# Optimization experiments

Hardware: AMD Instinct MI355X
Metric: run time of the kernel (lower is better)

Reference implementation:

```python
import jax, jax.numpy as jnp
import numpy as np

N, D, H, G = 262144, 256, 8, 2048
DH = D // H  # 32


def setup_inputs() -> dict:
    key = jax.random.key(0)
    ks = jax.random.split(key, 12)
    s = 0.02
    x = jax.random.normal(ks[0], (N, D), jnp.float32)
    # equal-size sets: batch[i] = set id, ptr = CSR boundaries (consistent pair)
    batch = jnp.repeat(jnp.arange(G, dtype=jnp.int64), N // G)
    ptr = jnp.arange(G + 1, dtype=jnp.int64) * (N // G)
    rn = lambda k, sh: jax.random.normal(k, sh, jnp.float32) * s
    return {
        "x": x, "ptr": ptr, "batch": batch,
        "lin_w": rn(ks[1], (D, D)), "lin_b": jnp.zeros((D,), jnp.float32),
        "seed": rn(ks[2], (D,)),
        "wq": rn(ks[3], (D, D)), "bq": jnp.zeros((D,), jnp.float32),
        "wk": rn(ks[4], (D, D)), "bk": jnp.zeros((D,), jnp.float32),
        "wv": rn(ks[5], (D, D)), "bv": jnp.zeros((D,), jnp.float32),
        "wo": rn(ks[6], (D, D)), "bo": jnp.zeros((D,), jnp.float32),
        "mlp_w1": rn(ks[7], (D, D)), "mlp_b1": jnp.zeros((D,), jnp.float32),
        "mlp_w2": rn(ks[8], (D, D)), "mlp_b2": jnp.zeros((D,), jnp.float32),
    }


def gelu(v):
    return jax.nn.gelu(v, approximate=False)  # torch nn.GELU default (erf)


def reference(x, ptr, batch, lin_w, lin_b, seed, wq, bq, wk, bk, wv, bv,
              wo, bo, mlp_w1, mlp_b1, mlp_w2, mlp_b2):
    # pre-projection + GELU
    h = gelu(x @ lin_w + lin_b)                         # [N, D]
    # PMA-style multihead attention pooling over ragged sets
    q = (seed @ wq + bq).reshape(H, DH)                 # learnable seed query per head
    k = (h @ wk + bk).reshape(-1, H, DH)                # [N, H, DH]
    v = (h @ wv + bv).reshape(-1, H, DH)                # [N, H, DH]
    scores = jnp.einsum('nhd,hd->nh', k, q) / jnp.sqrt(jnp.float32(DH))  # [N, H]
    # segment (per-set) numerically-stable softmax
    m = jax.ops.segment_max(scores, batch, num_segments=G)   # [G, H]
    e = jnp.exp(scores - m[batch])
    z = jax.ops.segment_sum(e, batch, num_segments=G)        # [G, H]
    w = e / z[batch]                                         # [N, H] attention weights
    pooled = jax.ops.segment_sum(w[:, :, None] * v, batch, num_segments=G)  # [G, H, DH]
    pooled = pooled.reshape(G, D) @ wo + bo                  # output projection [G, D]
    # 2-layer MLP head (plain_last: no act on final layer; dropout=0 at eval)
    out = gelu(pooled @ mlp_w1 + mlp_b1) @ mlp_w2 + mlp_b2   # [G, D]
    return out
```

## Files before the change

kernel.cpp:

```cpp
#include <hip/hip_runtime.h>
#include <hip/hip_bf16.h>

#define DD 256
#define SETSZ 128
#define NSETS 2048

typedef __attribute__((ext_vector_type(8))) __bf16 bf16x8;
typedef __attribute__((ext_vector_type(8))) unsigned short u16x8;
typedef __attribute__((ext_vector_type(4))) float f32x4;

static __device__ __forceinline__ unsigned short f2bf(float f) {
    unsigned u = __builtin_bit_cast(unsigned, f);
    u += 0x7fffu + ((u >> 16) & 1u);
    return (unsigned short)(u >> 16);
}

static __device__ __forceinline__ float gelu_f(float v) {
    return 0.5f * v * (1.0f + erff(v * 0.70710678118654752f));
}

__global__ void prep1_kernel(const float* __restrict__ seed, const float* __restrict__ wq,
                             const float* __restrict__ bq, float* __restrict__ q) {
    int j = threadIdx.x;
    float s = bq[j];
#pragma unroll 16
    for (int d = 0; d < DD; ++d) s += seed[d] * wq[d * DD + j];
    q[j] = s;
}

__global__ void prep2_kernel(const float* __restrict__ lin_w, const float* __restrict__ wv,
                             const float* __restrict__ wk, const float* __restrict__ q,
                             unsigned short* __restrict__ linT, unsigned short* __restrict__ wvT,
                             unsigned short* __restrict__ wkqB) {
    int b = blockIdx.x, t = threadIdx.x;
    if (b < DD) {
        linT[b * DD + t] = f2bf(lin_w[t * DD + b]);
        wvT[b * DD + t]  = f2bf(wv[t * DD + b]);
    } else {
        const float inv = 0.17677669529663687f;
        for (int c = 0; c < 8; ++c) {
            float s = 0.f;
#pragma unroll 8
            for (int j = 0; j < 32; ++j) s += wk[t * DD + c * 32 + j] * q[c * 32 + j];
            wkqB[c * DD + t] = f2bf(s * inv);
        }
        for (int c = 8; c < 16; ++c) wkqB[c * DD + t] = 0;
    }
}

__global__ __launch_bounds__(512, 2)
void attn_pool_kernel(const float* __restrict__ x, const float* __restrict__ lin_b,
                      const float* __restrict__ bv,
                      const unsigned short* __restrict__ linT,
                      const unsigned short* __restrict__ wvT,
                      const unsigned short* __restrict__ wkqB,
                      float* __restrict__ pooled) {
    __shared__ unsigned short xs[SETSZ * DD];
    const int g = blockIdx.x;
    const int t = threadIdx.x;
    const int lane = t & 63;
    const int wid = t >> 6;
    const int l15 = lane & 15;
    const int kg = lane >> 4;
    const long r0 = (long)g * SETSZ;

#pragma unroll
    for (int i = 0; i < 8; ++i) {
        int c = i * 512 + t;
        int row = c >> 5;
        int cg = c & 31;
        const float4* src = reinterpret_cast<const float4*>(x + (r0 + row) * DD + cg * 8);
        float4 a0 = src[0];
        float4 a1 = src[1];
        u16x8 v;
        v[0] = f2bf(a0.x); v[1] = f2bf(a0.y); v[2] = f2bf(a0.z); v[3] = f2bf(a0.w);
        v[4] = f2bf(a1.x); v[5] = f2bf(a1.y); v[6] = f2bf(a1.z); v[7] = f2bf(a1.w);
        int sg = cg ^ (row & 7);
        *reinterpret_cast<u16x8*>(&xs[row * DD + sg * 8]) = v;
    }
    __syncthreads();

    const int colbase = wid * 32;

    f32x4 acc[8][2];
#pragma unroll
    for (int r = 0; r < 8; ++r) { acc[r][0] = 0.f; acc[r][1] = 0.f; }

#pragma unroll
    for (int ks = 0; ks < 8; ++ks) {
        bf16x8 af[8];
#pragma unroll
        for (int r = 0; r < 8; ++r) {
            int row = r * 16 + l15;
            int sg = (ks * 4 + kg) ^ (row & 7);
            af[r] = *reinterpret_cast<const bf16x8*>(&xs[row * DD + sg * 8]);
        }
        int bofs = ks * 32 + kg * 8;
        bf16x8 b0 = *reinterpret_cast<const bf16x8*>(linT + (colbase + l15) * DD + bofs);
        bf16x8 b1 = *reinterpret_cast<const bf16x8*>(linT + (colbase + 16 + l15) * DD + bofs);
#pragma unroll
        for (int r = 0; r < 8; ++r) {
            acc[r][0] = __builtin_amdgcn_mfma_f32_16x16x32_bf16(af[r], b0, acc[r][0], 0, 0, 0);
            acc[r][1] = __builtin_amdgcn_mfma_f32_16x16x32_bf16(af[r], b1, acc[r][1], 0, 0, 0);
        }
    }
    __syncthreads();

    {
        float lb0 = lin_b[colbase + l15];
        float lb1 = lin_b[colbase + 16 + l15];
#pragma unroll
        for (int r = 0; r < 8; ++r) {
#pragma unroll
            for (int c = 0; c < 2; ++c) {
                int col = colbase + c * 16 + l15;
                float lb = c ? lb1 : lb0;
#pragma unroll
                for (int j = 0; j < 4; ++j) {
                    int row = r * 16 + kg * 4 + j;
                    float hv = gelu_f(acc[r][c][j] + lb);
                    int sg = (col >> 3) ^ (row & 7);
                    xs[row * DD + sg * 8 + (col & 7)] = f2bf(hv);
                }
            }
        }
    }
    __syncthreads();

    f32x4 vacc[8][2];
    f32x4 sacc[8];
#pragma unroll
    for (int r = 0; r < 8; ++r) { vacc[r][0] = 0.f; vacc[r][1] = 0.f; sacc[r] = 0.f; }

#pragma unroll
    for (int ks = 0; ks < 8; ++ks) {
        bf16x8 af[8];
#pragma unroll
        for (int r = 0; r < 8; ++r) {
            int row = r * 16 + l15;
            int sg = (ks * 4 + kg) ^ (row & 7);
            af[r] = *reinterpret_cast<const bf16x8*>(&xs[row * DD + sg * 8]);
        }
        int bofs = ks * 32 + kg * 8;
        bf16x8 b0 = *reinterpret_cast<const bf16x8*>(wvT + (colbase + l15) * DD + bofs);
        bf16x8 b1 = *reinterpret_cast<const bf16x8*>(wvT + (colbase + 16 + l15) * DD + bofs);
        bf16x8 bq8 = *reinterpret_cast<const bf16x8*>(wkqB + l15 * DD + bofs);
#pragma unroll
        for (int r = 0; r < 8; ++r) {
            vacc[r][0] = __builtin_amdgcn_mfma_f32_16x16x32_bf16(af[r], b0, vacc[r][0], 0, 0, 0);
            vacc[r][1] = __builtin_amdgcn_mfma_f32_16x16x32_bf16(af[r], b1, vacc[r][1], 0, 0, 0);
            sacc[r]    = __builtin_amdgcn_mfma_f32_16x16x32_bf16(af[r], bq8, sacc[r], 0, 0, 0);
        }
    }

    float e[8][4];
    float mx = -1e30f;
#pragma unroll
    for (int r = 0; r < 8; ++r)
#pragma unroll
        for (int j = 0; j < 4; ++j) {
            float s = __shfl(sacc[r][j], (lane & 48) | wid, 64);
            e[r][j] = s;
            mx = fmaxf(mx, s);
        }
    mx = fmaxf(mx, __shfl_xor(mx, 16, 64));
    mx = fmaxf(mx, __shfl_xor(mx, 32, 64));
    float z = 0.f;
#pragma unroll
    for (int r = 0; r < 8; ++r)
#pragma unroll
        for (int j = 0; j < 4; ++j) {
            float ee = __expf(e[r][j] - mx);
            e[r][j] = ee;
            z += ee;
        }
    z += __shfl_xor(z, 16, 64);
    z += __shfl_xor(z, 32, 64);
    float inv = 1.0f / z;

#pragma unroll
    for (int c = 0; c < 2; ++c) {
        float pp = 0.f;
#pragma unroll
        for (int r = 0; r < 8; ++r)
#pragma unroll
            for (int j = 0; j < 4; ++j) pp += e[r][j] * vacc[r][c][j];
        pp *= inv;
        pp += __shfl_xor(pp, 16, 64);
        pp += __shfl_xor(pp, 32, 64);
        if (kg == 0) {
            int col = colbase + c * 16 + l15;
            pooled[(long)g * DD + col] = pp + bv[col];
        }
    }
}

__global__ __launch_bounds__(256)
void mlp_kernel(const float* __restrict__ pooled,
                const float* __restrict__ wo, const float* __restrict__ bo,
                const float* __restrict__ w1, const float* __restrict__ b1,
                const float* __restrict__ w2, const float* __restrict__ b2,
                float* __restrict__ out) {
    __shared__ float sa[8][DD];
    __shared__ float sb[8][DD];
    const int c = threadIdx.x;
    const long base = (long)blockIdx.x * 8 * DD;
#pragma unroll
    for (int r = 0; r < 8; ++r) sa[r][c] = pooled[base + r * DD + c];
    __syncthreads();
    {
        float acc[8];
        float bb = bo[c];
#pragma unroll
        for (int r = 0; r < 8; ++r) acc[r] = bb;
#pragma unroll 4
        for (int k = 0; k < DD; ++k) {
            float wvv = wo[k * DD + c];
#pragma unroll
            for (int r = 0; r < 8; ++r) acc[r] += sa[r][k] * wvv;
        }
#pragma unroll
        for (int r = 0; r < 8; ++r) sb[r][c] = acc[r];
    }
    __syncthreads();
    {
        float acc[8];
        float bb = b1[c];
#pragma unroll
        for (int r = 0; r < 8; ++r) acc[r] = bb;
#pragma unroll 4
        for (int k = 0; k < DD; ++k) {
            float wvv = w1[k * DD + c];
#pragma unroll
            for (int r = 0; r < 8; ++r) acc[r] += sb[r][k] * wvv;
        }
#pragma unroll
        for (int r = 0; r < 8; ++r) sa[r][c] = gelu_f(acc[r]);
    }
    __syncthreads();
    {
        float acc[8];
        float bb = b2[c];
#pragma unroll
        for (int r = 0; r < 8; ++r) acc[r] = bb;
#pragma unroll 4
        for (int k = 0; k < DD; ++k) {
            float wvv = w2[k * DD + c];
#pragma unroll
            for (int r = 0; r < 8; ++r) acc[r] += sa[r][k] * wvv;
        }
#pragma unroll
        for (int r = 0; r < 8; ++r) out[base + r * DD + c] = acc[r];
    }
}

extern "C" void kernel_launch(void* const* d_in, const int* in_sizes, int n_in,
                              void* d_out, int out_size, void* d_ws, size_t ws_size,
                              hipStream_t stream) {
    const float* x     = (const float*)d_in[0];
    const float* lin_w = (const float*)d_in[3];
    const float* lin_b = (const float*)d_in[4];
    const float* seed  = (const float*)d_in[5];
    const float* wq    = (const float*)d_in[6];
    const float* bq    = (const float*)d_in[7];
    const float* wk    = (const float*)d_in[8];
    const float* wvp   = (const float*)d_in[10];
    const float* bv    = (const float*)d_in[11];
    const float* wo    = (const float*)d_in[12];
    const float* bo    = (const float*)d_in[13];
    const float* w1    = (const float*)d_in[14];
    const float* b1    = (const float*)d_in[15];
    const float* w2    = (const float*)d_in[16];
    const float* b2    = (const float*)d_in[17];
    float* out = (float*)d_out;

    char* ws = (char*)d_ws;
    float* q             = (float*)ws;
    unsigned short* wkqB = (unsigned short*)(ws + 4096);
    unsigned short* linT = (unsigned short*)(ws + 16384);
    unsigned short* wvT  = (unsigned short*)(ws + 16384 + 131072);
    float* pooled        = (float*)(ws + 16384 + 262144);

    prep1_kernel<<<1, 256, 0, stream>>>(seed, wq, bq, q);
    prep2_kernel<<<257, 256, 0, stream>>>(lin_w, wvp, wk, q, linT, wvT, wkqB);
    attn_pool_kernel<<<NSETS, 512, 0, stream>>>(x, lin_b, bv, linT, wvT, wkqB, pooled);
    mlp_kernel<<<NSETS / 8, 256, 0, stream>>>(pooled, wo, bo, w1, b1, w2, b2, out);
}
```

Baseline: 250.7 us.

## Tile attention-pool over 32-row chunks with online softmax and register prefetch

The attention-pool kernel now processes each 128-row set in four 32-row tiles instead of staging the whole set in LDS. The 64 KB LDS buffer shrinks to 16 KB, and launch bounds rise to allow 6 blocks per CU. Each tile accumulates the softmax with a running max and rescaling (online softmax), and the next tile's x is prefetched into registers while the current tile computes. In exchange the kernel does more barriers per block, runs a smaller MFMA batch per iteration, and exposes load latency per tile. It also uses an extra XOR term in the LDS swizzle.

```diff
diff --git a/kernel.cpp b/kernel.cpp
--- a/kernel.cpp
+++ b/kernel.cpp
@@ -3,6 +3,8 @@
 
 #define DD 256
 #define SETSZ 128
+#define TROWS 32
+#define NTILES 4
 #define NSETS 2048
 
 typedef __attribute__((ext_vector_type(8))) __bf16 bf16x8;
@@ -17,6 +19,10 @@
 
 static __device__ __forceinline__ float gelu_f(float v) {
     return 0.5f * v * (1.0f + erff(v * 0.70710678118654752f));
+}
+
+static __device__ __forceinline__ int swz(int row, int cg) {
+    return cg ^ (row & 7) ^ ((row >> 3) & 3);
 }
 
 __global__ void prep1_kernel(const float* __restrict__ seed, const float* __restrict__ wq,
@@ -48,14 +54,14 @@
     }
 }
 
-__global__ __launch_bounds__(512, 2)
+__global__ __launch_bounds__(512, 6)
 void attn_pool_kernel(const float* __restrict__ x, const float* __restrict__ lin_b,
                       const float* __restrict__ bv,
                       const unsigned short* __restrict__ linT,
                       const unsigned short* __restrict__ wvT,
                       const unsigned short* __restrict__ wkqB,
                       float* __restrict__ pooled) {
-    __shared__ unsigned short xs[SETSZ * DD];
+    __shared__ unsigned short xs[TROWS * DD];
     const int g = blockIdx.x;
     const int t = threadIdx.x;
     const int lane = t & 63;
@@ -63,135 +69,162 @@
     const int l15 = lane & 15;
     const int kg = lane >> 4;
     const long r0 = (long)g * SETSZ;
-
-#pragma unroll
-    for (int i = 0; i < 8; ++i) {
-        int c = i * 512 + t;
-        int row = c >> 5;
-        int cg = c & 31;
-        const float4* src = reinterpret_cast<const float4*>(x + (r0 + row) * DD + cg * 8);
-        float4 a0 = src[0];
-        float4 a1 = src[1];
-        u16x8 v;
-        v[0] = f2bf(a0.x); v[1] = f2bf(a0.y); v[2] = f2bf(a0.z); v[3] = f2bf(a0.w);
-        v[4] = f2bf(a1.x); v[5] = f2bf(a1.y); v[6] = f2bf(a1.z); v[7] = f2bf(a1.w);
-        int sg = cg ^ (row & 7);
-        *reinterpret_cast<u16x8*>(&xs[row * DD + sg * 8]) = v;
+    const int colbase = wid * 32;
+
+    const int srow0 = t >> 5;
+    const int srow1 = srow0 + 16;
+    const int scg = t & 31;
+    const int soff0 = srow0 * DD + swz(srow0, scg) * 8;
+    const int soff1 = srow1 * DD + swz(srow1, scg) * 8;
+
+    const float lb0 = lin_b[colbase + l15];
+    const float lb1 = lin_b[colbase + 16 + l15];
+
+    float m = -1e30f, z = 0.f, pp0 = 0.f, pp1 = 0.f;
+
+    {
+        const float* p0 = x + (r0 + srow0) * DD + scg * 8;
+        const float* p1 = x + (r0 + srow1) * DD + scg * 8;
+        float4 a0 = *(const float4*)p0;
+        float4 a1 = *(const float4*)(p0 + 4);
+        float4 c0 = *(const float4*)p1;
+        float4 c1 = *(const float4*)(p1 + 4);
+        u16x8 v0, v1;
+        v0[0]=f2bf(a0.x); v0[1]=f2bf(a0.y); v0[2]=f2bf(a0.z); v0[3]=f2bf(a0.w);
+        v0[4]=f2bf(a1.x); v0[5]=f2bf(a1.y); v0[6]=f2bf(a1.z); v0[7]=f2bf(a1.w);
+        v1[0]=f2bf(c0.x); v1[1]=f2bf(c0.y); v1[2]=f2bf(c0.z); v1[3]=f2bf(c0.w);
+        v1[4]=f2bf(c1.x); v1[5]=f2bf(c1.y); v1[6]=f2bf(c1.z); v1[7]=f2bf(c1.w);
+        *reinterpret_cast<u16x8*>(&xs[soff0]) = v0;
+        *reinterpret_cast<u16x8*>(&xs[soff1]) = v1;
     }
     __syncthreads();
 
-    const int colbase = wid * 32;
-
-    f32x4 acc[8][2];
-#pragma unroll
-    for (int r = 0; r < 8; ++r) { acc[r][0] = 0.f; acc[r][1] = 0.f; }
-
-#pragma unroll
-    for (int ks = 0; ks < 8; ++ks) {
-        bf16x8 af[8];
-#pragma unroll
-        for (int r = 0; r < 8; ++r) {
-            int row = r * 16 + l15;
-            int sg = (ks * 4 + kg) ^ (row & 7);
-            af[r] = *reinterpret_cast<const bf16x8*>(&xs[row * DD + sg * 8]);
-        }
-        int bofs = ks * 32 + kg * 8;
-        bf16x8 b0 = *reinterpret_cast<const bf16x8*>(linT + (colbase + l15) * DD + bofs);
-        bf16x8 b1 = *reinterpret_cast<const bf16x8*>(linT + (colbase + 16 + l15) * DD + bofs);
-#pragma unroll
-        for (int r = 0; r < 8; ++r) {
-            acc[r][0] = __builtin_amdgcn_mfma_f32_16x16x32_bf16(af[r], b0, acc[r][0], 0, 0, 0);
-            acc[r][1] = __builtin_amdgcn_mfma_f32_16x16x32_bf16(af[r], b1, acc[r][1], 0, 0, 0);
-        }
-    }
-    __syncthreads();
-
-    {
-        float lb0 = lin_b[colbase + l15];
-        float lb1 = lin_b[colbase + 16 + l15];
-#pragma unroll
-        for (int r = 0; r < 8; ++r) {
+#pragma unroll 1
+    for (int tl = 0; tl < NTILES; ++tl) {
+        float4 pf0, pf1, pf2, pf3;
+        if (tl < NTILES - 1) {
+            const float* p0 = x + (r0 + (tl + 1) * TROWS + srow0) * DD + scg * 8;
+            const float* p1 = x + (r0 + (tl + 1) * TROWS + srow1) * DD + scg * 8;
+            pf0 = *(const float4*)p0;
+            pf1 = *(const float4*)(p0 + 4);
+            pf2 = *(const float4*)p1;
+            pf3 = *(const float4*)(p1 + 4);
+        }
+
+        f32x4 acc[2][2];
+        acc[0][0] = 0.f; acc[0][1] = 0.f; acc[1][0] = 0.f; acc[1][1] = 0.f;
+#pragma unroll 2
+        for (int ks = 0; ks < 8; ++ks) {
+            bf16x8 af[2];
+#pragma unroll
+            for (int rr = 0; rr < 2; ++rr) {
+                int row = rr * 16 + l15;
+                af[rr] = *reinterpret_cast<const bf16x8*>(&xs[row * DD + swz(row, ks * 4 + kg) * 8]);
+            }
+            int bofs = ks * 32 + kg * 8;
+            bf16x8 b0 = *reinterpret_cast<const bf16x8*>(linT + (colbase + l15) * DD + bofs);
+            bf16x8 b1 = *reinterpret_cast<const bf16x8*>(linT + (colbase + 16 + l15) * DD + bofs);
+#pragma unroll
+            for (int rr = 0; rr < 2; ++rr) {
+                acc[rr][0] = __builtin_amdgcn_mfma_f32_16x16x32_bf16(af[rr], b0, acc[rr][0], 0, 0, 0);
+                acc[rr][1] = __builtin_amdgcn_mfma_f32_16x16x32_bf16(af[rr], b1, acc[rr][1], 0, 0, 0);
+            }
+        }
+        __syncthreads();
+
+#pragma unroll
+        for (int rr = 0; rr < 2; ++rr) {
 #pragma unroll
             for (int c = 0; c < 2; ++c) {
                 int col = colbase + c * 16 + l15;
                 float lb = c ? lb1 : lb0;
 #pragma unroll
                 for (int j = 0; j < 4; ++j) {
-                    int row = r * 16 + kg * 4 + j;
-                    float hv = gelu_f(acc[r][c][j] + lb);
-                    int sg = (col >> 3) ^ (row & 7);
-                    xs[row * DD + sg * 8 + (col & 7)] = f2bf(hv);
+                    int row = rr * 16 + kg * 4 + j;
+                    float hv = gelu_f(acc[rr][c][j] + lb);
+                    xs[row * DD + swz(row, col >> 3) * 8 + (col & 7)] = f2bf(hv);
                 }
             }
         }
-    }
-    __syncthreads();
-
-    f32x4 vacc[8][2];
-    f32x4 sacc[8];
-#pragma unroll
-    for (int r = 0; r < 8; ++r) { vacc[r][0] = 0.f; vacc[r][1] = 0.f; sacc[r] = 0.f; }
-
-#pragma unroll
-    for (int ks = 0; ks < 8; ++ks) {
-        bf16x8 af[8];
-#pragma unroll
-        for (int r = 0; r < 8; ++r) {
-            int row = r * 16 + l15;
-            int sg = (ks * 4 + kg) ^ (row & 7);
-            af[r] = *reinterpret_cast<const bf16x8*>(&xs[row * DD + sg * 8]);
-        }
-        int bofs = ks * 32 + kg * 8;
-        bf16x8 b0 = *reinterpret_cast<const bf16x8*>(wvT + (colbase + l15) * DD + bofs);
-        bf16x8 b1 = *reinterpret_cast<const bf16x8*>(wvT + (colbase + 16 + l15) * DD + bofs);
-        bf16x8 bq8 = *reinterpret_cast<const bf16x8*>(wkqB + l15 * DD + bofs);
-#pragma unroll
-        for (int r = 0; r < 8; ++r) {
-            vacc[r][0] = __builtin_amdgcn_mfma_f32_16x16x32_bf16(af[r], b0, vacc[r][0], 0, 0, 0);
-            vacc[r][1] = __builtin_amdgcn_mfma_f32_16x16x32_bf16(af[r], b1, vacc[r][1], 0, 0, 0);
-            sacc[r]    = __builtin_amdgcn_mfma_f32_16x16x32_bf16(af[r], bq8, sacc[r], 0, 0, 0);
-        }
-    }
-
-    float e[8][4];
-    float mx = -1e30f;
-#pragma unroll
-    for (int r = 0; r < 8; ++r)
-#pragma unroll
-        for (int j = 0; j < 4; ++j) {
-            float s = __shfl(sacc[r][j], (lane & 48) | wid, 64);
-            e[r][j] = s;
-            mx = fmaxf(mx, s);
-        }
-    mx = fmaxf(mx, __shfl_xor(mx, 16, 64));
-    mx = fmaxf(mx, __shfl_xor(mx, 32, 64));
-    float z = 0.f;
-#pragma unroll
-    for (int r = 0; r < 8; ++r)
-#pragma unroll
-        for (int j = 0; j < 4; ++j) {
-            float ee = __expf(e[r][j] - mx);
-            e[r][j] = ee;
-            z += ee;
-        }
+        __syncthreads();
+
+        f32x4 vacc[2][2];
+        f32x4 sacc[2];
+        vacc[0][0] = 0.f; vacc[0][1] = 0.f; vacc[1][0] = 0.f; vacc[1][1] = 0.f;
+        sacc[0] = 0.f; sacc[1] = 0.f;
+#pragma unroll 2
+        for (int ks = 0; ks < 8; ++ks) {
+            bf16x8 af[2];
+#pragma unroll
+            for (int rr = 0; rr < 2; ++rr) {
+                int row = rr * 16 + l15;
+                af[rr] = *reinterpret_cast<const bf16x8*>(&xs[row * DD + swz(row, ks * 4 + kg) * 8]);
+            }
+            int bofs = ks * 32 + kg * 8;
+            bf16x8 b0  = *reinterpret_cast<const bf16x8*>(wvT + (colbase + l15) * DD + bofs);
+            bf16x8 b1  = *reinterpret_cast<const bf16x8*>(wvT + (colbase + 16 + l15) * DD + bofs);
+            bf16x8 bq8 = *reinterpret_cast<const bf16x8*>(wkqB + l15 * DD + bofs);
+#pragma unroll
+            for (int rr = 0; rr < 2; ++rr) {
+                vacc[rr][0] = __builtin_amdgcn_mfma_f32_16x16x32_bf16(af[rr], b0, vacc[rr][0], 0, 0, 0);
+                vacc[rr][1] = __builtin_amdgcn_mfma_f32_16x16x32_bf16(af[rr], b1, vacc[rr][1], 0, 0, 0);
+                sacc[rr]    = __builtin_amdgcn_mfma_f32_16x16x32_bf16(af[rr], bq8, sacc[rr], 0, 0, 0);
+            }
+        }
+        __syncthreads();
+
+        {
+            float sv[2][4];
+            float tm = -1e30f;
+#pragma unroll
+            for (int rr = 0; rr < 2; ++rr)
+#pragma unroll
+                for (int j = 0; j < 4; ++j) {
+                    float s = __shfl(sacc[rr][j], (lane & 48) | wid, 64);
+                    sv[rr][j] = s;
+                    tm = fmaxf(tm, s);
+                }
+            tm = fmaxf(tm, __shfl_xor(tm, 16, 64));
+            tm = fmaxf(tm, __shfl_xor(tm, 32, 64));
+            float mnew = fmaxf(m, tm);
+            float al = __expf(m - mnew);
+            z *= al; pp0 *= al; pp1 *= al;
+#pragma unroll
+            for (int rr = 0; rr < 2; ++rr)
+#pragma unroll
+                for (int j = 0; j < 4; ++j) {
+                    float e = __expf(sv[rr][j] - mnew);
+                    z += e;
+                    pp0 += e * vacc[rr][0][j];
+                    pp1 += e * vacc[rr][1][j];
+                }
+            m = mnew;
+        }
+
+        if (tl < NTILES - 1) {
+            u16x8 v0, v1;
+            v0[0]=f2bf(pf0.x); v0[1]=f2bf(pf0.y); v0[2]=f2bf(pf0.z); v0[3]=f2bf(pf0.w);
+            v0[4]=f2bf(pf1.x); v0[5]=f2bf(pf1.y); v0[6]=f2bf(pf1.z); v0[7]=f2bf(pf1.w);
+            v1[0]=f2bf(pf2.x); v1[1]=f2bf(pf2.y); v1[2]=f2bf(pf2.z); v1[3]=f2bf(pf2.w);
+            v1[4]=f2bf(pf3.x); v1[5]=f2bf(pf3.y); v1[6]=f2bf(pf3.z); v1[7]=f2bf(pf3.w);
+            *reinterpret_cast<u16x8*>(&xs[soff0]) = v0;
+            *reinterpret_cast<u16x8*>(&xs[soff1]) = v1;
+        }
+        __syncthreads();
+    }
+
     z += __shfl_xor(z, 16, 64);
     z += __shfl_xor(z, 32, 64);
+    pp0 += __shfl_xor(pp0, 16, 64);
+    pp0 += __shfl_xor(pp0, 32, 64);
+    pp1 += __shfl_xor(pp1, 16, 64);
+    pp1 += __shfl_xor(pp1, 32, 64);
     float inv = 1.0f / z;
-
-#pragma unroll
-    for (int c = 0; c < 2; ++c) {
-        float pp = 0.f;
-#pragma unroll
-        for (int r = 0; r < 8; ++r)
-#pragma unroll
-            for (int j = 0; j < 4; ++j) pp += e[r][j] * vacc[r][c][j];
-        pp *= inv;
-        pp += __shfl_xor(pp, 16, 64);
-        pp += __shfl_xor(pp, 32, 64);
-        if (kg == 0) {
-            int col = colbase + c * 16 + l15;
-            pooled[(long)g * DD + col] = pp + bv[col];
-        }
+    if (kg == 0) {
+        int c0 = colbase + l15;
+        int c1 = colbase + 16 + l15;
+        pooled[(long)g * DD + c0] = pp0 * inv + bv[c0];
+        pooled[(long)g * DD + c1] = pp1 * inv + bv[c1];
     }
 }
 
```

Result: slower. 525.7 us (+109.7%).

## Make attention-pool kernel persistent with double-buffered LDS and register prefetch

Applied to the files above, without the earlier changes.

Launches 256 persistent blocks, each processing 8 sets in sequence. While the MFMAs for the current set run, each block loads the next set's x into registers and writes it as bf16 into a second LDS buffer, so global loads overlap compute. The LDS swizzle also gains an extra XOR term to reduce bank conflicts. In exchange, doubling LDS to 128 KB per block drops residency to one block per CU, and the prefetch registers add pressure under the existing launch bounds, which may cause spills.

```diff
diff --git a/kernel.cpp b/kernel.cpp
--- a/kernel.cpp
+++ b/kernel.cpp
@@ -4,6 +4,8 @@
 #define DD 256
 #define SETSZ 128
 #define NSETS 2048
+#define NBLK 256
+#define SPB (NSETS / NBLK)
 
 typedef __attribute__((ext_vector_type(8))) __bf16 bf16x8;
 typedef __attribute__((ext_vector_type(8))) unsigned short u16x8;
@@ -18,6 +20,15 @@
 static __device__ __forceinline__ float gelu_f(float v) {
     return 0.5f * v * (1.0f + erff(v * 0.70710678118654752f));
 }
+
+static __device__ __forceinline__ int swz(int row, int cg) {
+    return cg ^ (row & 7) ^ ((row >> 3) & 3);
+}
+
+#define LGKM_BARRIER() do { \
+    asm volatile("s_waitcnt lgkmcnt(0)" ::: "memory"); \
+    __builtin_amdgcn_s_barrier(); \
+} while (0)
 
 __global__ void prep1_kernel(const float* __restrict__ seed, const float* __restrict__ wq,
                              const float* __restrict__ bq, float* __restrict__ q) {
@@ -55,143 +66,183 @@
                       const unsigned short* __restrict__ wvT,
                       const unsigned short* __restrict__ wkqB,
                       float* __restrict__ pooled) {
-    __shared__ unsigned short xs[SETSZ * DD];
-    const int g = blockIdx.x;
+    __shared__ unsigned short bufs[2][SETSZ * DD];
     const int t = threadIdx.x;
     const int lane = t & 63;
     const int wid = t >> 6;
     const int l15 = lane & 15;
     const int kg = lane >> 4;
-    const long r0 = (long)g * SETSZ;
-
-#pragma unroll
-    for (int i = 0; i < 8; ++i) {
-        int c = i * 512 + t;
-        int row = c >> 5;
-        int cg = c & 31;
-        const float4* src = reinterpret_cast<const float4*>(x + (r0 + row) * DD + cg * 8);
-        float4 a0 = src[0];
-        float4 a1 = src[1];
+    const int colbase = wid * 32;
+    const long set0 = (long)blockIdx.x * SPB;
+
+    const float lb0 = lin_b[colbase + l15];
+    const float lb1 = lin_b[colbase + 16 + l15];
+
+    auto issueg = [&](const float* nb, int g, float4* pr) {
+        const float4* src = reinterpret_cast<const float4*>(nb);
+        int c0 = g * 2048 + 2 * t;
+        pr[0] = src[c0];
+        pr[1] = src[c0 + 1];
+        pr[2] = src[c0 + 1024];
+        pr[3] = src[c0 + 1025];
+    };
+    auto writeg = [&](unsigned short* dst, int g, const float4* pr) {
+        int c0 = g * 2048 + 2 * t;
+        int row = c0 >> 6;
+        int cg = (c0 & 63) >> 1;
         u16x8 v;
-        v[0] = f2bf(a0.x); v[1] = f2bf(a0.y); v[2] = f2bf(a0.z); v[3] = f2bf(a0.w);
-        v[4] = f2bf(a1.x); v[5] = f2bf(a1.y); v[6] = f2bf(a1.z); v[7] = f2bf(a1.w);
-        int sg = cg ^ (row & 7);
-        *reinterpret_cast<u16x8*>(&xs[row * DD + sg * 8]) = v;
-    }
-    __syncthreads();
-
-    const int colbase = wid * 32;
-
-    f32x4 acc[8][2];
-#pragma unroll
-    for (int r = 0; r < 8; ++r) { acc[r][0] = 0.f; acc[r][1] = 0.f; }
-
-#pragma unroll
-    for (int ks = 0; ks < 8; ++ks) {
-        bf16x8 af[8];
-#pragma unroll
-        for (int r = 0; r < 8; ++r) {
-            int row = r * 16 + l15;
-            int sg = (ks * 4 + kg) ^ (row & 7);
-            af[r] = *reinterpret_cast<const bf16x8*>(&xs[row * DD + sg * 8]);
-        }
-        int bofs = ks * 32 + kg * 8;
-        bf16x8 b0 = *reinterpret_cast<const bf16x8*>(linT + (colbase + l15) * DD + bofs);
-        bf16x8 b1 = *reinterpret_cast<const bf16x8*>(linT + (colbase + 16 + l15) * DD + bofs);
-#pragma unroll
-        for (int r = 0; r < 8; ++r) {
-            acc[r][0] = __builtin_amdgcn_mfma_f32_16x16x32_bf16(af[r], b0, acc[r][0], 0, 0, 0);
-            acc[r][1] = __builtin_amdgcn_mfma_f32_16x16x32_bf16(af[r], b1, acc[r][1], 0, 0, 0);
-        }
-    }
-    __syncthreads();
+        v[0] = f2bf(pr[0].x); v[1] = f2bf(pr[0].y); v[2] = f2bf(pr[0].z); v[3] = f2bf(pr[0].w);
+        v[4] = f2bf(pr[1].x); v[5] = f2bf(pr[1].y); v[6] = f2bf(pr[1].z); v[7] = f2bf(pr[1].w);
+        *reinterpret_cast<u16x8*>(&dst[row * DD + swz(row, cg) * 8]) = v;
+        int row2 = row + 16;
+        u16x8 w;
+        w[0] = f2bf(pr[2].x); w[1] = f2bf(pr[2].y); w[2] = f2bf(pr[2].z); w[3] = f2bf(pr[2].w);
+        w[4] = f2bf(pr[3].x); w[5] = f2bf(pr[3].y); w[6] = f2bf(pr[3].z); w[7] = f2bf(pr[3].w);
+        *reinterpret_cast<u16x8*>(&dst[row2 * DD + swz(row2, cg) * 8]) = w;
+    };
 
     {
-        float lb0 = lin_b[colbase + l15];
-        float lb1 = lin_b[colbase + 16 + l15];
-#pragma unroll
-        for (int r = 0; r < 8; ++r) {
+        const float* nb = x + set0 * SETSZ * DD;
+        float4 pr[4];
+#pragma unroll
+        for (int g = 0; g < 4; ++g) { issueg(nb, g, pr); writeg(bufs[0], g, pr); }
+    }
+    LGKM_BARRIER();
+
+    int cur = 0;
+    for (int s = 0; s < SPB; ++s) {
+        const unsigned short* xc = bufs[cur];
+        unsigned short* xcm = bufs[cur];
+        unsigned short* xn = bufs[cur ^ 1];
+        const bool pf = (s + 1 < SPB);
+        const float* nb = x + (set0 + s + 1) * SETSZ * DD;
+        float4 p0[4], p1[4], p2[4], p3[4];
+
+        f32x4 acc[8][2];
+#pragma unroll
+        for (int rr = 0; rr < 8; ++rr) { acc[rr][0] = 0.f; acc[rr][1] = 0.f; }
+
+        if (pf) { issueg(nb, 0, p0); issueg(nb, 1, p1); }
+#pragma unroll
+        for (int ks = 0; ks < 4; ++ks) {
+            int bofs = ks * 32 + kg * 8;
+            bf16x8 b0 = *reinterpret_cast<const bf16x8*>(linT + (colbase + l15) * DD + bofs);
+            bf16x8 b1 = *reinterpret_cast<const bf16x8*>(linT + (colbase + 16 + l15) * DD + bofs);
+#pragma unroll
+            for (int rr = 0; rr < 8; ++rr) {
+                int row = rr * 16 + l15;
+                bf16x8 a = *reinterpret_cast<const bf16x8*>(&xc[row * DD + swz(row, ks * 4 + kg) * 8]);
+                acc[rr][0] = __builtin_amdgcn_mfma_f32_16x16x32_bf16(a, b0, acc[rr][0], 0, 0, 0);
+                acc[rr][1] = __builtin_amdgcn_mfma_f32_16x16x32_bf16(a, b1, acc[rr][1], 0, 0, 0);
+            }
+        }
+        if (pf) issueg(nb, 2, p2);
+#pragma unroll
+        for (int ks = 4; ks < 8; ++ks) {
+            int bofs = ks * 32 + kg * 8;
+            bf16x8 b0 = *reinterpret_cast<const bf16x8*>(linT + (colbase + l15) * DD + bofs);
+            bf16x8 b1 = *reinterpret_cast<const bf16x8*>(linT + (colbase + 16 + l15) * DD + bofs);
+#pragma unroll
+            for (int rr = 0; rr < 8; ++rr) {
+                int row = rr * 16 + l15;
+                bf16x8 a = *reinterpret_cast<const bf16x8*>(&xc[row * DD + swz(row, ks * 4 + kg) * 8]);
+                acc[rr][0] = __builtin_amdgcn_mfma_f32_16x16x32_bf16(a, b0, acc[rr][0], 0, 0, 0);
+                acc[rr][1] = __builtin_amdgcn_mfma_f32_16x16x32_bf16(a, b1, acc[rr][1], 0, 0, 0);
+            }
+        }
+        if (pf) issueg(nb, 3, p3);
+        LGKM_BARRIER();
+
+#pragma unroll
+        for (int rr = 0; rr < 8; ++rr) {
 #pragma unroll
             for (int c = 0; c < 2; ++c) {
                 int col = colbase + c * 16 + l15;
                 float lb = c ? lb1 : lb0;
 #pragma unroll
                 for (int j = 0; j < 4; ++j) {
-                    int row = r * 16 + kg * 4 + j;
-                    float hv = gelu_f(acc[r][c][j] + lb);
-                    int sg = (col >> 3) ^ (row & 7);
-                    xs[row * DD + sg * 8 + (col & 7)] = f2bf(hv);
+                    int row = rr * 16 + kg * 4 + j;
+                    float hv = gelu_f(acc[rr][c][j] + lb);
+                    xcm[row * DD + swz(row, col >> 3) * 8 + (col & 7)] = f2bf(hv);
                 }
             }
         }
-    }
-    __syncthreads();
-
-    f32x4 vacc[8][2];
-    f32x4 sacc[8];
-#pragma unroll
-    for (int r = 0; r < 8; ++r) { vacc[r][0] = 0.f; vacc[r][1] = 0.f; sacc[r] = 0.f; }
-
-#pragma unroll
-    for (int ks = 0; ks < 8; ++ks) {
-        bf16x8 af[8];
-#pragma unroll
-        for (int r = 0; r < 8; ++r) {
-            int row = r * 16 + l15;
-            int sg = (ks * 4 + kg) ^ (row & 7);
-            af[r] = *reinterpret_cast<const bf16x8*>(&xs[row * DD + sg * 8]);
-        }
-        int bofs = ks * 32 + kg * 8;
-        bf16x8 b0 = *reinterpret_cast<const bf16x8*>(wvT + (colbase + l15) * DD + bofs);
-        bf16x8 b1 = *reinterpret_cast<const bf16x8*>(wvT + (colbase + 16 + l15) * DD + bofs);
-        bf16x8 bq8 = *reinterpret_cast<const bf16x8*>(wkqB + l15 * DD + bofs);
-#pragma unroll
-        for (int r = 0; r < 8; ++r) {
-            vacc[r][0] = __builtin_amdgcn_mfma_f32_16x16x32_bf16(af[r], b0, vacc[r][0], 0, 0, 0);
-            vacc[r][1] = __builtin_amdgcn_mfma_f32_16x16x32_bf16(af[r], b1, vacc[r][1], 0, 0, 0);
-            sacc[r]    = __builtin_amdgcn_mfma_f32_16x16x32_bf16(af[r], bq8, sacc[r], 0, 0, 0);
-        }
-    }
-
-    float e[8][4];
-    float mx = -1e30f;
-#pragma unroll
-    for (int r = 0; r < 8; ++r)
-#pragma unroll
-        for (int j = 0; j < 4; ++j) {
-            float s = __shfl(sacc[r][j], (lane & 48) | wid, 64);
-            e[r][j] = s;
-            mx = fmaxf(mx, s);
-        }
-    mx = fmaxf(mx, __shfl_xor(mx, 16, 64));
-    mx = fmaxf(mx, __shfl_xor(mx, 32, 64));
-    float z = 0.f;
-#pragma unroll
-    for (int r = 0; r < 8; ++r)
-#pragma unroll
-        for (int j = 0; j < 4; ++j) {
-            float ee = __expf(e[r][j] - mx);
-            e[r][j] = ee;
-            z += ee;
-        }
-    z += __shfl_xor(z, 16, 64);
-    z += __shfl_xor(z, 32, 64);
-    float inv = 1.0f / z;
-
-#pragma unroll
-    for (int c = 0; c < 2; ++c) {
-        float pp = 0.f;
-#pragma unroll
-        for (int r = 0; r < 8; ++r)
-#pragma unroll
-            for (int j = 0; j < 4; ++j) pp += e[r][j] * vacc[r][c][j];
-        pp *= inv;
-        pp += __shfl_xor(pp, 16, 64);
-        pp += __shfl_xor(pp, 32, 64);
-        if (kg == 0) {
-            int col = colbase + c * 16 + l15;
-            pooled[(long)g * DD + col] = pp + bv[col];
-        }
+        LGKM_BARRIER();
+
+        f32x4 vacc[8][2];
+        f32x4 sacc[8];
+#pragma unroll
+        for (int rr = 0; rr < 8; ++rr) { vacc[rr][0] = 0.f; vacc[rr][1] = 0.f; sacc[rr] = 0.f; }
+
+#pragma unroll
+        for (int ksb = 0; ksb < 4; ++ksb) {
+#pragma unroll
+            for (int ki = 0; ki < 2; ++ki) {
+                int ks = ksb * 2 + ki;
+                int bofs = ks * 32 + kg * 8;
+                bf16x8 b0  = *reinterpret_cast<const bf16x8*>(wvT + (colbase + l15) * DD + bofs);
+                bf16x8 b1  = *reinterpret_cast<const bf16x8*>(wvT + (colbase + 16 + l15) * DD + bofs);
+                bf16x8 bq8 = *reinterpret_cast<const bf16x8*>(wkqB + l15 * DD + bofs);
+#pragma unroll
+                for (int rr = 0; rr < 8; ++rr) {
+                    int row = rr * 16 + l15;
+                    bf16x8 a = *reinterpret_cast<const bf16x8*>(&xc[row * DD + swz(row, ks * 4 + kg) * 8]);
+                    vacc[rr][0] = __builtin_amdgcn_mfma_f32_16x16x32_bf16(a, b0, vacc[rr][0], 0, 0, 0);
+                    vacc[rr][1] = __builtin_amdgcn_mfma_f32_16x16x32_bf16(a, b1, vacc[rr][1], 0, 0, 0);
+                    sacc[rr]    = __builtin_amdgcn_mfma_f32_16x16x32_bf16(a, bq8, sacc[rr], 0, 0, 0);
+                }
+            }
+            if (pf) {
+                if (ksb == 0) writeg(xn, 0, p0);
+                else if (ksb == 1) writeg(xn, 1, p1);
+                else if (ksb == 2) writeg(xn, 2, p2);
+                else writeg(xn, 3, p3);
+            }
+        }
+
+        float e[8][4];
+        float mx = -1e30f;
+#pragma unroll
+        for (int rr = 0; rr < 8; ++rr)
+#pragma unroll
+            for (int j = 0; j < 4; ++j) {
+                float sv = __shfl(sacc[rr][j], (lane & 48) | wid, 64);
+                e[rr][j] = sv;
+                mx = fmaxf(mx, sv);
+            }
+        mx = fmaxf(mx, __shfl_xor(mx, 16, 64));
+        mx = fmaxf(mx, __shfl_xor(mx, 32, 64));
+        float z = 0.f;
+#pragma unroll
+        for (int rr = 0; rr < 8; ++rr)
+#pragma unroll
+            for (int j = 0; j < 4; ++j) {
+                float ee = __expf(e[rr][j] - mx);
+                e[rr][j] = ee;
+                z += ee;
+            }
+        z += __shfl_xor(z, 16, 64);
+        z += __shfl_xor(z, 32, 64);
+        float inv = 1.0f / z;
+
+#pragma unroll
+        for (int c = 0; c < 2; ++c) {
+            float pp = 0.f;
+#pragma unroll
+            for (int rr = 0; rr < 8; ++rr)
+#pragma unroll
+                for (int j = 0; j < 4; ++j) pp += e[rr][j] * vacc[rr][c][j];
+            pp *= inv;
+            pp += __shfl_xor(pp, 16, 64);
+            pp += __shfl_xor(pp, 32, 64);
+            if (kg == 0) {
+                int col = colbase + c * 16 + l15;
+                pooled[(set0 + s) * DD + col] = pp + bv[col];
+            }
+        }
+
+        LGKM_BARRIER();
+        cur ^= 1;
     }
 }
 
@@ -283,6 +334,6 @@
 
     prep1_kernel<<<1, 256, 0, stream>>>(seed, wq, bq, q);
     prep2_kernel<<<257, 256, 0, stream>>>(lin_w, wvp, wk, q, linT, wvT, wkqB);
-    attn_pool_kernel<<<NSETS, 512, 0, stream>>>(x, lin_b, bv, linT, wvT, wkqB, pooled);
+    attn_pool_kernel<<<NBLK, 512, 0, stream>>>(x, lin_b, bv, linT, wvT, wkqB, pooled);
     mlp_kernel<<<NSETS / 8, 256, 0, stream>>>(pooled, wo, bo, w1, b1, w2, b2, out);
 }
```

After: 632.0 us. 152% more time.
